# Performance work log

Measured on AMD Instinct MI355X. Metric: run time of the kernel, lower is better.

Reference implementation:

```python
import jax, jax.numpy as jnp
import numpy as np

N, D = 4096, 1024
DH = D // 2  # head=2 (forced by the two-way chunk unpack in the source)
W_SCALE = 0.02


def setup_inputs() -> dict:
    key = jax.random.key(0)
    ks = jax.random.split(key, 7)
    mk = lambda k: jax.random.normal(k, (DH, DH), dtype=jnp.float32) * W_SCALE
    return {
        "x": jax.random.normal(ks[0], (N, D), dtype=jnp.float32),
        "Wq1": mk(ks[1]), "Wq2": mk(ks[2]),
        "Wk1": mk(ks[3]), "Wk2": mk(ks[4]),
        "Wv1": mk(ks[5]), "Wv2": mk(ks[6]),
    }


def _head(xh, Wq, Wk, Wv):
    # xh: (Dh, N) channel-major chunk, W*: (Dh, Dh) 1x1-conv weights
    q = Wq @ xh  # (Dh, N)
    k = Wk @ xh  # (Dh, N)
    v = Wv @ xh  # (Dh, N)
    # QK_T conv: Sc[i, j] = k_i . q_j ; permuted -> S[j, i] = q_j . k_i
    S = jnp.einsum("dn,dm->nm", q, k)  # (N, N), no softmax / no 1/sqrt(Dh) in source
    # Sc_V conv with S as weight: out[j, d] = sum_i S[j, i] * v[d, i]
    return jnp.einsum("nm,dm->nd", S, v)  # (N, Dh)


def reference(x, Wq1, Wq2, Wk1, Wk2, Wv1, Wv2):
    xT = x.T  # (D, N), matches x.permute(1,0).reshape(D, N, 1)
    x1, x2 = xT[:DH], xT[DH:]
    o1 = _head(x1, Wq1, Wk1, Wv1)
    o2 = _head(x2, Wq2, Wk2, Wv2)
    return jnp.concatenate([o1, o2], axis=1)  # (N, D), matches concat+squeeze
```

## Files before the change

kernel.cpp:

```cpp
#include <hip/hip_runtime.h>
#include <hip/hip_bf16.h>

#define N_ROWS 4096
#define D_FULL 1024
#define DHALF  512
#define GSPLIT 16

typedef __attribute__((ext_vector_type(8))) short bf16x8;
typedef __attribute__((ext_vector_type(8))) unsigned short u16x8;
typedef __attribute__((ext_vector_type(4))) float f32x4;

__device__ __forceinline__ unsigned short f2b(float f) {
  __hip_bfloat16 h = __float2bfloat16(f);
  union { __hip_bfloat16 b; unsigned short u; } cv;
  cv.b = h;
  return cv.u;
}
__device__ __forceinline__ float b2f(unsigned short u) {
  union { unsigned int i; float f; } cv;
  cv.i = ((unsigned int)u) << 16;
  return cv.f;
}

__device__ __forceinline__ void load_lds16(const void* g, void* l) {
  __builtin_amdgcn_global_load_lds(
      (const __attribute__((address_space(1))) unsigned int*)g,
      (__attribute__((address_space(3))) unsigned int*)l, 16, 0, 0);
}

template<int N> __device__ __forceinline__ void vmwait() {
  if constexpr (N == 0)       asm volatile("s_waitcnt vmcnt(0)" ::: "memory");
  else if constexpr (N == 3)  asm volatile("s_waitcnt vmcnt(3)" ::: "memory");
  else if constexpr (N == 4)  asm volatile("s_waitcnt vmcnt(4)" ::: "memory");
  else if constexpr (N == 6)  asm volatile("s_waitcnt vmcnt(6)" ::: "memory");
  else if constexpr (N == 8)  asm volatile("s_waitcnt vmcnt(8)" ::: "memory");
  else                        asm volatile("s_waitcnt vmcnt(16)" ::: "memory");
}
__device__ __forceinline__ void barx() {
  __builtin_amdgcn_sched_barrier(0);
  __builtin_amdgcn_s_barrier();
  __builtin_amdgcn_sched_barrier(0);
}
__device__ __forceinline__ int b3inc(int b) { return b == 2 ? 0 : b + 1; }

__device__ __forceinline__ void cvt_tile(const float* __restrict__ src, int lds_,
                                         unsigned short* __restrict__ dst, int ldd,
                                         unsigned short* __restrict__ dstT, int ldt,
                                         int n0, int c0) {
  __shared__ unsigned short tile[64][66];
  const int t  = threadIdx.x;
  const int r  = t >> 2;
  const int cq = (t & 3) * 16;

  unsigned short loc[16];
  #pragma unroll
  for (int i = 0; i < 4; ++i) {
    float4 v = *reinterpret_cast<const float4*>(&src[(size_t)(n0 + r) * lds_ + c0 + cq + i * 4]);
    loc[i*4+0] = f2b(v.x); loc[i*4+1] = f2b(v.y); loc[i*4+2] = f2b(v.z); loc[i*4+3] = f2b(v.w);
  }
  if (dst) {
    u16x8 a, b;
    #pragma unroll
    for (int i = 0; i < 8; ++i) { a[i] = loc[i]; b[i] = loc[8+i]; }
    unsigned short* p = &dst[(size_t)(n0 + r) * ldd + c0 + cq];
    *reinterpret_cast<u16x8*>(p)     = a;
    *reinterpret_cast<u16x8*>(p + 8) = b;
  }
  if (dstT) {
    #pragma unroll
    for (int i = 0; i < 8; ++i) {
      ushort2 w2; w2.x = loc[2*i]; w2.y = loc[2*i+1];
      *reinterpret_cast<ushort2*>(&tile[r][cq + 2*i]) = w2;
    }
    __syncthreads();
    const int c  = t >> 2;
    const int ng = (t & 3) * 16;
    unsigned short o[16];
    #pragma unroll
    for (int i = 0; i < 16; ++i) o[i] = tile[ng + i][c];
    u16x8 a, b;
    #pragma unroll
    for (int i = 0; i < 8; ++i) { a[i] = o[i]; b[i] = o[8+i]; }
    unsigned short* p = &dstT[(size_t)(c0 + c) * ldt + n0 + ng];
    *reinterpret_cast<u16x8*>(p)     = a;
    *reinterpret_cast<u16x8*>(p + 8) = b;
  }
}

__global__ __launch_bounds__(256) void k_cvt_all(const float* __restrict__ x,
                                                 const float* __restrict__ w0, const float* __restrict__ w1,
                                                 const float* __restrict__ w2, const float* __restrict__ w3,
                                                 const float* __restrict__ w4, const float* __restrict__ w5,
                                                 unsigned short* __restrict__ xb,
                                                 unsigned short* __restrict__ xT,
                                                 unsigned short* __restrict__ Wb,
                                                 unsigned short* __restrict__ WbT) {
  const int b = blockIdx.x;
  if (b < 1024) {
    cvt_tile(x, D_FULL, xb, D_FULL, xT, N_ROWS, (b >> 4) * 64, (b & 15) * 64);
  } else {
    const int b2 = b - 1024;
    const int z = b2 >> 6, t = b2 & 63;
    const float* w;
    switch (z) {
      case 0: w = w0; break; case 1: w = w1; break; case 2: w = w2; break;
      case 3: w = w3; break; case 4: w = w4; break; default: w = w5; break;
    }
    const size_t HH = (size_t)DHALF * DHALF;
    unsigned short* d  = (z >= 4) ? (Wb  + z * HH) : nullptr;
    unsigned short* dT = (z <  4) ? (WbT + z * HH) : nullptr;
    cvt_tile(w, DHALF, d, DHALF, dT, DHALF, (t >> 3) * 64, (t & 7) * 64);
  }
}

__global__ __launch_bounds__(256) void k_gp(const unsigned short* __restrict__ xT,
                                            const unsigned short* __restrict__ WbT,
                                            unsigned short* __restrict__ Gp,
                                            unsigned short* __restrict__ P) {
  const int o   = blockIdx.x + blockIdx.y * 4 + blockIdx.z * 16;
  const int swz = (o & 7) * 68 + (o >> 3);
  const int bx = swz & 3, by = (swz >> 2) & 3, bz = swz >> 4;

  const unsigned short* Ab;
  const unsigned short* Bb;
  unsigned short* Cb;
  int lda, nt;
  const long long HH = 262144;
  if (bz < 2) {
    const int h = bz;
    Ab = WbT + (size_t)h * HH;
    Bb = WbT + (size_t)(2 + h) * HH;
    Cb = P + (size_t)h * HH;
    lda = DHALF; nt = DHALF >> 5;
  } else {
    const int zz = bz - 2;
    const int h = zz >> 4, s = zz & 15;
    Ab = xT + (size_t)h * DHALF * N_ROWS + s * (N_ROWS / GSPLIT);
    Bb = Ab;
    Cb = Gp + (size_t)zz * HH;
    lda = N_ROWS; nt = (N_ROWS / GSPLIT) >> 5;
  }
  const int n0 = bx * 128;
  const int m0 = by * 128;

  __shared__ __align__(16) unsigned short lds[3][2][128 * 32];

  const int tid  = threadIdx.x;
  const int lane = tid & 63;
  const int wave = tid >> 6;
  const int wm = (wave >> 1) * 64;
  const int wn = (wave & 1) * 64;
  const int fr = lane & 15;
  const int kg = (lane >> 4) * 8;

  const int srow = wave * 32 + (lane >> 2);
  const int scol = (lane & 3) * 8;
  const unsigned short* gA0 = Ab + (size_t)(m0 + srow) * lda + scol;
  const unsigned short* gA1 = gA0 + (size_t)16 * lda;
  const unsigned short* gB0 = Bb + (size_t)(n0 + srow) * lda + scol;
  const unsigned short* gB1 = gB0 + (size_t)16 * lda;
  const int stOff = wave * 1024;

  f32x4 acc[4][4] = {};

  auto STAGE = [&](int buf, int t) {
    const int kofs = t * 32;
    load_lds16(gA0 + kofs, &lds[buf][0][stOff]);
    load_lds16(gA1 + kofs, &lds[buf][0][stOff + 512]);
    load_lds16(gB0 + kofs, &lds[buf][1][stOff]);
    load_lds16(gB1 + kofs, &lds[buf][1][stOff + 512]);
  };
  auto COMPUTE = [&](int buf) {
    const unsigned short* la = &lds[buf][0][0];
    const unsigned short* lb = &lds[buf][1][0];
    bf16x8 af[4], bf[4];
    #pragma unroll
    for (int f = 0; f < 4; ++f) {
      af[f] = *reinterpret_cast<const bf16x8*>(&la[(wm + f * 16 + fr) * 32 + kg]);
      bf[f] = *reinterpret_cast<const bf16x8*>(&lb[(wn + f * 16 + fr) * 32 + kg]);
    }
    #pragma unroll
    for (int fm = 0; fm < 4; ++fm)
      #pragma unroll
      for (int fn = 0; fn < 4; ++fn)
        acc[fm][fn] = __builtin_amdgcn_mfma_f32_16x16x32_bf16(af[fm], bf[fn], acc[fm][fn], 0, 0, 0);
  };

  STAGE(0, 0); STAGE(1, 1);
  int bufS = 2, bufC = 0;
  for (int t = 0; t < nt - 2; ++t) {
    STAGE(bufS, t + 2); bufS = b3inc(bufS);
    vmwait<8>(); barx();
    COMPUTE(bufC); bufC = b3inc(bufC);
    barx();
  }
  vmwait<4>(); barx();
  COMPUTE(bufC); bufC = b3inc(bufC);
  vmwait<0>(); barx();
  COMPUTE(bufC);

  #pragma unroll
  for (int fm = 0; fm < 4; ++fm)
    #pragma unroll
    for (int fn = 0; fn < 4; ++fn)
      #pragma unroll
      for (int r = 0; r < 4; ++r) {
        int row = m0 + wm + fm * 16 + (lane >> 4) * 4 + r;
        int col = n0 + wn + fn * 16 + fr;
        Cb[(size_t)row * DHALF + col] = f2b(acc[fm][fn][r]);
      }
}

__global__ __launch_bounds__(256) void k_gred(const unsigned short* __restrict__ Gp,
                                              unsigned short* __restrict__ G) {
  int gid = blockIdx.x * 256 + threadIdx.x;
  int h = gid >> 15;
  size_t e = (size_t)(gid & 32767) * 8;
  size_t base = (size_t)h * GSPLIT * (DHALF * DHALF) + e;
  float sum[8] = {};
  #pragma unroll
  for (int s = 0; s < GSPLIT; ++s) {
    u16x8 v = *reinterpret_cast<const u16x8*>(&Gp[base + (size_t)s * (DHALF * DHALF)]);
    #pragma unroll
    for (int i = 0; i < 8; ++i) sum[i] += b2f(v[i]);
  }
  u16x8 o;
  #pragma unroll
  for (int i = 0; i < 8; ++i) o[i] = f2b(sum[i]);
  *reinterpret_cast<u16x8*>(&G[(size_t)h * (DHALF * DHALF) + e]) = o;
}

__global__ __launch_bounds__(256) void k_s(const unsigned short* __restrict__ A,
                                           const unsigned short* __restrict__ B,
                                           unsigned short* __restrict__ C,
                                           long long hA, long long hB, long long hC) {
  const int o   = blockIdx.x + blockIdx.y * 8 + blockIdx.z * 64;
  const int swz = (o & 7) * 16 + (o >> 3);
  const int bx = swz & 7, by = (swz >> 3) & 7, bz = swz >> 6;

  const unsigned short* Ab = A + (size_t)bz * hA;
  const unsigned short* Bb = B + (size_t)bz * hB;
  unsigned short* Cb = C + (size_t)bz * hC;
  const int n0 = bx * 64;
  const int m0 = by * 64;

  __shared__ __align__(16) unsigned short lds[3][2][4][64 * 32];

  const int tid  = threadIdx.x;
  const int lane = tid & 63;
  const int wave = tid >> 6;
  const int wm = (wave >> 1) * 32;
  const int wn = (wave & 1) * 32;
  const int fr = lane & 15;
  const int kg = (lane >> 4) * 8;

  const int srow = lane >> 2;
  const int scol = (lane & 3) * 8;
  const unsigned short* gA = Ab + (size_t)(m0 + srow) * DHALF + wave * 32 + scol;
  const unsigned short* gB = Bb + (size_t)(n0 + srow) * DHALF + wave * 32 + scol;

  f32x4 acc[2][2] = {};

  auto STAGE = [&](int buf, int t) {
    const int kofs = t * 128;
    #pragma unroll
    for (int j = 0; j < 4; ++j) {
      load_lds16(gA + kofs + j * 16 * DHALF, &lds[buf][0][wave][j * 512]);
      load_lds16(gB + kofs + j * 16 * DHALF, &lds[buf][1][wave][j * 512]);
    }
  };
  auto COMPUTE = [&](int buf) {
    #pragma unroll
    for (int p = 0; p < 4; ++p) {
      bf16x8 a0 = *reinterpret_cast<const bf16x8*>(&lds[buf][0][p][(wm + fr) * 32 + kg]);
      bf16x8 a1 = *reinterpret_cast<const bf16x8*>(&lds[buf][0][p][(wm + 16 + fr) * 32 + kg]);
      bf16x8 b0 = *reinterpret_cast<const bf16x8*>(&lds[buf][1][p][(wn + fr) * 32 + kg]);
      bf16x8 b1 = *reinterpret_cast<const bf16x8*>(&lds[buf][1][p][(wn + 16 + fr) * 32 + kg]);
      acc[0][0] = __builtin_amdgcn_mfma_f32_16x16x32_bf16(a0, b0, acc[0][0], 0, 0, 0);
      acc[0][1] = __builtin_amdgcn_mfma_f32_16x16x32_bf16(a0, b1, acc[0][1], 0, 0, 0);
      acc[1][0] = __builtin_amdgcn_mfma_f32_16x16x32_bf16(a1, b0, acc[1][0], 0, 0, 0);
      acc[1][1] = __builtin_amdgcn_mfma_f32_16x16x32_bf16(a1, b1, acc[1][1], 0, 0, 0);
    }
  };

  STAGE(0, 0); STAGE(1, 1);
  int bufS = 2, bufC = 0;
  for (int t = 0; t < 2; ++t) {
    STAGE(bufS, t + 2); bufS = b3inc(bufS);
    vmwait<16>(); barx();
    COMPUTE(bufC); bufC = b3inc(bufC);
    barx();
  }
  vmwait<8>(); barx();
  COMPUTE(bufC); bufC = b3inc(bufC);
  vmwait<0>(); barx();
  COMPUTE(bufC);

  #pragma unroll
  for (int fm = 0; fm < 2; ++fm)
    #pragma unroll
    for (int fn = 0; fn < 2; ++fn)
      #pragma unroll
      for (int r = 0; r < 4; ++r) {
        int row = m0 + wm + fm * 16 + (lane >> 4) * 4 + r;
        int col = n0 + wn + fn * 16 + fr;
        Cb[(size_t)row * DHALF + col] = f2b(acc[fm][fn][r]);
      }
}

__global__ __launch_bounds__(256) void k_final(const unsigned short* __restrict__ xb,
                                               const unsigned short* __restrict__ MT,
                                               float* __restrict__ out) {
  const int o   = blockIdx.x + blockIdx.y * 8 + blockIdx.z * 256;
  const int swz = (o & 7) * 64 + (o >> 3);
  const int bx = swz & 7, by = (swz >> 3) & 31, bz = swz >> 8;

  const unsigned short* MTh = MT + (size_t)bz * 262144;
  const int hoff = bz * DHALF;
  const int n0 = bx * 64;
  const int m0 = by * 128;

  __shared__ __align__(16) unsigned short SH[3][6144];

  const int tid  = threadIdx.x;
  const int lane = tid & 63;
  const int wave = tid >> 6;
  const int wm = (wave >> 1) * 64;
  const int wn = (wave & 1) * 32;
  const int fr = lane & 15;
  const int kg = (lane >> 4) * 8;

  const int srow = wave * 32 + (lane >> 2);
  const int scol = (lane & 3) * 8;
  const unsigned short* gA0 = xb + (size_t)(m0 + srow) * D_FULL + hoff + scol;
  const unsigned short* gA1 = gA0 + (size_t)16 * D_FULL;
  const int brow = wave * 16 + (lane >> 2);
  const unsigned short* gB = MTh + (size_t)(n0 + brow) * DHALF + scol;

  f32x4 acc[4][2] = {};

  auto STAGE = [&](int buf, int t) {
    const int kofs = t * 32;
    unsigned short* Abuf = &SH[buf][0];
    unsigned short* Bbuf = &SH[buf][4096];
    load_lds16(gA0 + kofs, Abuf + wave * 1024);
    load_lds16(gA1 + kofs, Abuf + wave * 1024 + 512);
    load_lds16(gB + kofs, Bbuf + wave * 512);
  };
  auto COMPUTE = [&](int buf) {
    unsigned short* Abuf = &SH[buf][0];
    unsigned short* Bbuf = &SH[buf][4096];
    bf16x8 af[4], bv[2];
    #pragma unroll
    for (int f = 0; f < 4; ++f)
      af[f] = *reinterpret_cast<const bf16x8*>(&Abuf[(wm + f * 16 + fr) * 32 + kg]);
    #pragma unroll
    for (int f = 0; f < 2; ++f)
      bv[f] = *reinterpret_cast<const bf16x8*>(&Bbuf[(wn + f * 16 + fr) * 32 + kg]);
    #pragma unroll
    for (int fm = 0; fm < 4; ++fm)
      #pragma unroll
      for (int fn = 0; fn < 2; ++fn)
        acc[fm][fn] = __builtin_amdgcn_mfma_f32_16x16x32_bf16(af[fm], bv[fn], acc[fm][fn], 0, 0, 0);
  };

  STAGE(0, 0); STAGE(1, 1);
  int bufS = 2, bufC = 0;
  for (int t = 0; t < 14; ++t) {
    STAGE(bufS, t + 2); bufS = b3inc(bufS);
    vmwait<6>(); barx();
    COMPUTE(bufC); bufC = b3inc(bufC);
    barx();
  }
  vmwait<3>(); barx();
  COMPUTE(bufC); bufC = b3inc(bufC);
  vmwait<0>(); barx();
  COMPUTE(bufC);

  #pragma unroll
  for (int fm = 0; fm < 4; ++fm)
    #pragma unroll
    for (int fn = 0; fn < 2; ++fn)
      #pragma unroll
      for (int r = 0; r < 4; ++r) {
        int row = m0 + wm + fm * 16 + (lane >> 4) * 4 + r;
        int col = hoff + n0 + wn + fn * 16 + fr;
        out[(size_t)row * D_FULL + col] = acc[fm][fn][r];
      }
}

extern "C" void kernel_launch(void* const* d_in, const int* in_sizes, int n_in,
                              void* d_out, int out_size, void* d_ws, size_t ws_size,
                              hipStream_t stream) {
  const float* x   = (const float*)d_in[0];
  const float* Wq1 = (const float*)d_in[1];
  const float* Wq2 = (const float*)d_in[2];
  const float* Wk1 = (const float*)d_in[3];
  const float* Wk2 = (const float*)d_in[4];
  const float* Wv1 = (const float*)d_in[5];
  const float* Wv2 = (const float*)d_in[6];
  float* out = (float*)d_out;

  unsigned short* ws  = (unsigned short*)d_ws;
  unsigned short* xb  = ws;
  unsigned short* xT  = ws + 4194304;
  unsigned short* Wb  = ws + 8388608;
  unsigned short* WbT = ws + 9961472;
  unsigned short* G   = ws + 11534336;
  unsigned short* P   = ws + 12058624;
  unsigned short* TT  = ws + 12582912;
  unsigned short* MT  = ws + 13107200;
  unsigned short* Gp  = ws + 13631488;

  const long long HH = 262144;

  k_cvt_all<<<1408, 256, 0, stream>>>(x, Wq1, Wq2, Wk1, Wk2, Wv1, Wv2, xb, xT, Wb, WbT);

  k_gp<<<dim3(4, 4, 34), 256, 0, stream>>>(xT, WbT, Gp, P);

  k_gred<<<256, 256, 0, stream>>>(Gp, G);

  k_s<<<dim3(8, 8, 2), 256, 0, stream>>>(Wb + 4 * HH, G, TT, HH, HH, HH);
  k_s<<<dim3(8, 8, 2), 256, 0, stream>>>(TT, P, MT, HH, HH, HH);

  k_final<<<dim3(8, 32, 2), 256, 0, stream>>>(xb, MT, out);
}
```

Baseline: 50.43 us.

## Exploit Gram matrix symmetry: compute only upper-triangle tiles and mirror in reduction

The Gram matrix x_h x_h^T is symmetric, so the partial-Gram kernel now computes only the 10 upper-triangle 128x128 tiles per split instead of all 16. That cuts its work and partial-buffer writes by roughly a third. The grid is flattened to 352 blocks with a hand-built mapping that interleaves P-product tiles and Gram tiles across XCD groups. The reduction kernel now runs one block per output tile, reads the matching upper tile, and transposes it through LDS for lower-triangle tiles. This leaves only 32 reduction blocks, each holding 64 floats per thread, which risks low parallelism and high register pressure.

```diff
diff --git a/kernel.cpp b/kernel.cpp
--- a/kernel.cpp
+++ b/kernel.cpp
@@ -117,31 +117,34 @@
                                             const unsigned short* __restrict__ WbT,
                                             unsigned short* __restrict__ Gp,
                                             unsigned short* __restrict__ P) {
-  const int o   = blockIdx.x + blockIdx.y * 4 + blockIdx.z * 16;
-  const int swz = (o & 7) * 68 + (o >> 3);
-  const int bx = swz & 3, by = (swz >> 2) & 3, bz = swz >> 4;
+  const int o = blockIdx.x;
+  const int c = o & 7, j = o >> 3;
 
   const unsigned short* Ab;
   const unsigned short* Bb;
   unsigned short* Cb;
-  int lda, nt;
+  int lda, nt, m0, n0;
   const long long HH = 262144;
-  if (bz < 2) {
-    const int h = bz;
+  if (j < 4) {
+    const int pp = c * 4 + j;
+    const int h = pp >> 4, tile = pp & 15;
     Ab = WbT + (size_t)h * HH;
     Bb = WbT + (size_t)(2 + h) * HH;
     Cb = P + (size_t)h * HH;
-    lda = DHALF; nt = DHALF >> 5;
+    lda = DHALF; nt = 16;
+    m0 = (tile >> 2) * 128; n0 = (tile & 3) * 128;
   } else {
-    const int zz = bz - 2;
-    const int h = zz >> 4, s = zz & 15;
+    const int g = c * 40 + (j - 4);
+    const int slice = g / 10, p = g - slice * 10;
+    const int h = slice >> 4, s = slice & 15;
+    const int ti = (p < 4) ? 0 : (p < 7) ? 1 : (p < 9) ? 2 : 3;
+    const int tj = (p < 4) ? p : (p < 7) ? p - 3 : (p < 9) ? p - 5 : 3;
     Ab = xT + (size_t)h * DHALF * N_ROWS + s * (N_ROWS / GSPLIT);
     Bb = Ab;
-    Cb = Gp + (size_t)zz * HH;
-    lda = N_ROWS; nt = (N_ROWS / GSPLIT) >> 5;
-  }
-  const int n0 = bx * 128;
-  const int m0 = by * 128;
+    Cb = Gp + (size_t)slice * HH;
+    lda = N_ROWS; nt = 8;
+    m0 = ti * 128; n0 = tj * 128;
+  }
 
   __shared__ __align__(16) unsigned short lds[3][2][128 * 32];
 
@@ -213,21 +216,66 @@
 
 __global__ __launch_bounds__(256) void k_gred(const unsigned short* __restrict__ Gp,
                                               unsigned short* __restrict__ G) {
-  int gid = blockIdx.x * 256 + threadIdx.x;
-  int h = gid >> 15;
-  size_t e = (size_t)(gid & 32767) * 8;
-  size_t base = (size_t)h * GSPLIT * (DHALF * DHALF) + e;
-  float sum[8] = {};
-  #pragma unroll
+  __shared__ unsigned short S[128][132];
+  const int b = blockIdx.x;
+  const int h = b >> 4, tile = b & 15;
+  const int ti = tile >> 2, tj = tile & 3;
+  const bool lower = ti > tj;
+  const int sti = lower ? tj : ti;
+  const int stj = lower ? ti : tj;
+
+  const int t  = threadIdx.x;
+  const int r  = t >> 1;
+  const int ch = (t & 1) * 64;
+
+  const size_t HH = (size_t)DHALF * DHALF;
+  const size_t srcOff = (size_t)(sti * 128 + r) * DHALF + stj * 128 + ch;
+
+  float sum[64];
+  #pragma unroll
+  for (int i = 0; i < 64; ++i) sum[i] = 0.f;
   for (int s = 0; s < GSPLIT; ++s) {
-    u16x8 v = *reinterpret_cast<const u16x8*>(&Gp[base + (size_t)s * (DHALF * DHALF)]);
-    #pragma unroll
-    for (int i = 0; i < 8; ++i) sum[i] += b2f(v[i]);
-  }
-  u16x8 o;
-  #pragma unroll
-  for (int i = 0; i < 8; ++i) o[i] = f2b(sum[i]);
-  *reinterpret_cast<u16x8*>(&G[(size_t)h * (DHALF * DHALF) + e]) = o;
+    const unsigned short* p = Gp + ((size_t)(h * GSPLIT + s)) * HH + srcOff;
+    #pragma unroll
+    for (int k = 0; k < 8; ++k) {
+      u16x8 v = *reinterpret_cast<const u16x8*>(p + k * 8);
+      #pragma unroll
+      for (int i = 0; i < 8; ++i) sum[k * 8 + i] += b2f(v[i]);
+    }
+  }
+  unsigned short sb[64];
+  #pragma unroll
+  for (int i = 0; i < 64; ++i) sb[i] = f2b(sum[i]);
+
+  unsigned short* g = G + (size_t)h * HH;
+  if (!lower) {
+    unsigned short* p = g + (size_t)(ti * 128 + r) * DHALF + tj * 128 + ch;
+    #pragma unroll
+    for (int k = 0; k < 8; ++k) {
+      u16x8 ov;
+      #pragma unroll
+      for (int i = 0; i < 8; ++i) ov[i] = sb[k * 8 + i];
+      *reinterpret_cast<u16x8*>(p + k * 8) = ov;
+    }
+  } else {
+    #pragma unroll
+    for (int i = 0; i < 32; ++i) {
+      ushort2 w2; w2.x = sb[2*i]; w2.y = sb[2*i+1];
+      *reinterpret_cast<ushort2*>(&S[r][ch + 2*i]) = w2;
+    }
+    __syncthreads();
+    unsigned short ob[64];
+    #pragma unroll
+    for (int i = 0; i < 64; ++i) ob[i] = S[ch + i][r];
+    unsigned short* p = g + (size_t)(ti * 128 + r) * DHALF + tj * 128 + ch;
+    #pragma unroll
+    for (int k = 0; k < 8; ++k) {
+      u16x8 ov;
+      #pragma unroll
+      for (int i = 0; i < 8; ++i) ov[i] = ob[k * 8 + i];
+      *reinterpret_cast<u16x8*>(p + k * 8) = ov;
+    }
+  }
 }
 
 __global__ __launch_bounds__(256) void k_s(const unsigned short* __restrict__ A,
@@ -416,9 +464,9 @@
 
   k_cvt_all<<<1408, 256, 0, stream>>>(x, Wq1, Wq2, Wk1, Wk2, Wv1, Wv2, xb, xT, Wb, WbT);
 
-  k_gp<<<dim3(4, 4, 34), 256, 0, stream>>>(xT, WbT, Gp, P);
-
-  k_gred<<<256, 256, 0, stream>>>(Gp, G);
+  k_gp<<<352, 256, 0, stream>>>(xT, WbT, Gp, P);
+
+  k_gred<<<32, 256, 0, stream>>>(Gp, G);
 
   k_s<<<dim3(8, 8, 2), 256, 0, stream>>>(Wb + 4 * HH, G, TT, HH, HH, HH);
   k_s<<<dim3(8, 8, 2), 256, 0, stream>>>(TT, P, MT, HH, HH, HH);
```

After: 69.88 us. +38.6%, slower.

## Exploit Gram matrix symmetry: compute only upper-triangular tiles and mirror in reduction

Applied to the files above, without the earlier changes.

The partial Gram matrices x_h x_h^T are symmetric, so k_gp now computes only the 10 upper-triangular 128x128 tiles per slice instead of all 16, using a flat 352-block grid with a new XCD-aware block mapping. The reduction kernel k_gred fills the lower-triangular part by reading the transposed upper tile and transposing it through shared memory. This cuts GEMM work in the Gram stage by about 37%, at the cost of a more complex reduction with strided LDS transposes.

```diff
diff --git a/kernel.cpp b/kernel.cpp
--- a/kernel.cpp
+++ b/kernel.cpp
@@ -117,31 +117,34 @@
                                             const unsigned short* __restrict__ WbT,
                                             unsigned short* __restrict__ Gp,
                                             unsigned short* __restrict__ P) {
-  const int o   = blockIdx.x + blockIdx.y * 4 + blockIdx.z * 16;
-  const int swz = (o & 7) * 68 + (o >> 3);
-  const int bx = swz & 3, by = (swz >> 2) & 3, bz = swz >> 4;
+  const int o = blockIdx.x;
+  const int c = o & 7, j = o >> 3;
 
   const unsigned short* Ab;
   const unsigned short* Bb;
   unsigned short* Cb;
-  int lda, nt;
+  int lda, nt, m0, n0;
   const long long HH = 262144;
-  if (bz < 2) {
-    const int h = bz;
+  if (j < 4) {
+    const int pp = c * 4 + j;
+    const int h = pp >> 4, tile = pp & 15;
     Ab = WbT + (size_t)h * HH;
     Bb = WbT + (size_t)(2 + h) * HH;
     Cb = P + (size_t)h * HH;
-    lda = DHALF; nt = DHALF >> 5;
+    lda = DHALF; nt = 16;
+    m0 = (tile >> 2) * 128; n0 = (tile & 3) * 128;
   } else {
-    const int zz = bz - 2;
-    const int h = zz >> 4, s = zz & 15;
+    const int g = c * 40 + (j - 4);
+    const int slice = g / 10, p = g - slice * 10;
+    const int h = slice >> 4, s = slice & 15;
+    const int ti = (p < 4) ? 0 : (p < 7) ? 1 : (p < 9) ? 2 : 3;
+    const int tj = (p < 4) ? p : (p < 7) ? p - 3 : (p < 9) ? p - 5 : 3;
     Ab = xT + (size_t)h * DHALF * N_ROWS + s * (N_ROWS / GSPLIT);
     Bb = Ab;
-    Cb = Gp + (size_t)zz * HH;
-    lda = N_ROWS; nt = (N_ROWS / GSPLIT) >> 5;
-  }
-  const int n0 = bx * 128;
-  const int m0 = by * 128;
+    Cb = Gp + (size_t)slice * HH;
+    lda = N_ROWS; nt = 8;
+    m0 = ti * 128; n0 = tj * 128;
+  }
 
   __shared__ __align__(16) unsigned short lds[3][2][128 * 32];
 
@@ -213,21 +216,51 @@
 
 __global__ __launch_bounds__(256) void k_gred(const unsigned short* __restrict__ Gp,
                                               unsigned short* __restrict__ G) {
-  int gid = blockIdx.x * 256 + threadIdx.x;
-  int h = gid >> 15;
-  size_t e = (size_t)(gid & 32767) * 8;
-  size_t base = (size_t)h * GSPLIT * (DHALF * DHALF) + e;
-  float sum[8] = {};
-  #pragma unroll
-  for (int s = 0; s < GSPLIT; ++s) {
-    u16x8 v = *reinterpret_cast<const u16x8*>(&Gp[base + (size_t)s * (DHALF * DHALF)]);
-    #pragma unroll
-    for (int i = 0; i < 8; ++i) sum[i] += b2f(v[i]);
-  }
-  u16x8 o;
-  #pragma unroll
-  for (int i = 0; i < 8; ++i) o[i] = f2b(sum[i]);
-  *reinterpret_cast<u16x8*>(&G[(size_t)h * (DHALF * DHALF) + e]) = o;
+  __shared__ unsigned short T[32][66];
+  const int b   = blockIdx.x;
+  const int h   = b >> 7;
+  const int sub = b & 127;
+  const int sr  = sub >> 4, sc = sub & 15;
+  const int ti  = sr >> 1,  tj = sc >> 2;
+  const int t   = threadIdx.x;
+  const size_t HH = 262144;
+  const unsigned short* gpBase = Gp + (size_t)h * GSPLIT * HH;
+  unsigned short* g = G + (size_t)h * HH;
+
+  if (ti <= tj) {
+    const int r  = t >> 2;
+    const int cq = (t & 3) * 8;
+    const size_t off = (size_t)(sr * 64 + r) * DHALF + sc * 32 + cq;
+    float sum[8] = {};
+    for (int s = 0; s < GSPLIT; ++s) {
+      u16x8 v = *reinterpret_cast<const u16x8*>(gpBase + (size_t)s * HH + off);
+      #pragma unroll
+      for (int i = 0; i < 8; ++i) sum[i] += b2f(v[i]);
+    }
+    u16x8 o;
+    #pragma unroll
+    for (int i = 0; i < 8; ++i) o[i] = f2b(sum[i]);
+    *reinterpret_cast<u16x8*>(g + off) = o;
+  } else {
+    const int a  = t >> 3;
+    const int aq = (t & 7) * 8;
+    const size_t soff = (size_t)(sc * 32 + a) * DHALF + sr * 64 + aq;
+    float sum[8] = {};
+    for (int s = 0; s < GSPLIT; ++s) {
+      u16x8 v = *reinterpret_cast<const u16x8*>(gpBase + (size_t)s * HH + soff);
+      #pragma unroll
+      for (int i = 0; i < 8; ++i) sum[i] += b2f(v[i]);
+    }
+    #pragma unroll
+    for (int i = 0; i < 8; ++i) T[a][aq + i] = f2b(sum[i]);
+    __syncthreads();
+    const int r  = t >> 2;
+    const int cq = (t & 3) * 8;
+    u16x8 o;
+    #pragma unroll
+    for (int i = 0; i < 8; ++i) o[i] = T[cq + i][r];
+    *reinterpret_cast<u16x8*>(g + (size_t)(sr * 64 + r) * DHALF + sc * 32 + cq) = o;
+  }
 }
 
 __global__ __launch_bounds__(256) void k_s(const unsigned short* __restrict__ A,
@@ -416,7 +449,7 @@
 
   k_cvt_all<<<1408, 256, 0, stream>>>(x, Wq1, Wq2, Wk1, Wk2, Wv1, Wv2, xb, xT, Wb, WbT);
 
-  k_gp<<<dim3(4, 4, 34), 256, 0, stream>>>(xT, WbT, Gp, P);
+  k_gp<<<352, 256, 0, stream>>>(xT, WbT, Gp, P);
 
   k_gred<<<256, 256, 0, stream>>>(Gp, G);
 
```

Measured after the change: 49.01 us. -2.8%, faster.
